# Performance work log

Hardware: AMD Instinct MI355X
Metric: run time of the kernel (lower is better)

## Reference

```python
import jax, jax.numpy as jnp
import numpy as np

N, SD, VD, ED, E, NG, NA, NB = 512, 256, 128, 128, 262144, 16, 16, 5


def _lin_init(key, fan_in, fan_out):
    # torch.nn.Linear default: U(-1/sqrt(fan_in), 1/sqrt(fan_in)); stored as (in, out)
    lim = 1.0 / np.sqrt(fan_in)
    return jax.random.uniform(key, (fan_in, fan_out), jnp.float32, -lim, lim)


def setup_inputs() -> dict:
    key = jax.random.key(0)
    ks = jax.random.split(key, 20)
    s = jax.random.normal(ks[0], (N, SD), jnp.float32)
    v = jax.random.normal(ks[1], (N, 3, VD), jnp.float32)
    p = jax.random.normal(ks[2], (N, 3), jnp.float32)
    e = jax.random.normal(ks[3], (E, ED), jnp.float32)
    batch = jnp.sort(jax.random.randint(ks[4], (N,), 0, NG))
    edge_index_global = jax.random.randint(ks[5], (2, E), 0, N)
    W_sm = _lin_init(ks[6], SD, SD); b_sm = jnp.zeros((SD,), jnp.float32)
    W_bm = _lin_init(ks[7], ED, SD); b_bm = jnp.zeros((SD,), jnp.float32)
    W_b0 = _lin_init(ks[8], SD + 1, SD); b_b0 = jnp.zeros((SD,), jnp.float32)
    W_b1 = _lin_init(ks[9], SD, NB); b_b1 = jnp.zeros((NB,), jnp.float32)
    W_c = _lin_init(ks[10], VD, 1)  # no bias
    W_a = _lin_init(ks[11], SD, NA); b_a = jnp.zeros((NA,), jnp.float32)
    return {"s": s, "v": v, "p": p, "e": e, "batch": batch,
            "edge_index_global": edge_index_global,
            "W_sm": W_sm, "b_sm": b_sm, "W_bm": W_bm, "b_bm": b_bm,
            "W_b0": W_b0, "b_b0": b_b0, "W_b1": W_b1, "b_b1": b_b1,
            "W_c": W_c, "W_a": W_a, "b_a": b_a}


def reference(s, v, p, e, batch, edge_index_global,
              W_sm, b_sm, W_bm, b_bm, W_b0, b_b0, W_b1, b_b1, W_c, W_a, b_a):
    # shared_mapping: Linear + SiLU
    s = jax.nn.silu(s @ W_sm + b_sm)                      # [N, SD]
    coords_pred = (v @ W_c)[..., 0]                       # [N, 3]
    atoms_pred = s @ W_a + b_a                            # [N, NA]
    j, i = edge_index_global[0], edge_index_global[1]
    n = s.shape[0]
    # coords_param == 'data': coords = p + pred, then per-graph mean centering
    coords_pred = p + coords_pred
    seg_sum = jax.ops.segment_sum(coords_pred, batch, num_segments=NG)
    counts = jax.ops.segment_sum(jnp.ones((n, 1), coords_pred.dtype), batch, num_segments=NG)
    mean = seg_sum / jnp.maximum(counts, 1.0)
    coords_pred = coords_pred - mean[batch]
    # squared pairwise distance per edge
    d = jnp.sum((coords_pred[i] - coords_pred[j]) ** 2, axis=-1, keepdims=True)  # [E, 1]
    # sparse -> dense -> sparse symmetrization of edge features (as in the source)
    e_dense = jnp.zeros((n, n, e.shape[-1]), e.dtype).at[j, i].set(e)
    e_dense = 0.5 * (e_dense + jnp.transpose(e_dense, (1, 0, 2)))
    e_sym = e_dense[j, i]                                 # [E, ED]
    f = s[i] + s[j] + (e_sym @ W_bm + b_bm)               # [E, SD]
    edge = jnp.concatenate([f, d], axis=-1)               # [E, SD+1]
    bonds_pred = jax.nn.silu(edge @ W_b0 + b_b0) @ W_b1 + b_b1  # [E, NB]
    return coords_pred, atoms_pred, bonds_pred
```

## Files before the change

### kernel.cpp

```cpp
#include <hip/hip_runtime.h>
#include <math.h>

#define N_NODES 512
#define SD_ 256
#define VD_ 128
#define ED_ 128
#define NE_ 262144
#define NG_ 16
#define NA_ 16
#define NB_ 5
#define MAXP 131328

typedef __attribute__((ext_vector_type(8))) short bf16x8;
typedef __attribute__((ext_vector_type(4))) float f32x4;

__device__ __forceinline__ float silu_f(float x) { return x / (1.0f + expf(-x)); }
__device__ __forceinline__ float silu_fast(float x) {
    return x * __builtin_amdgcn_rcpf(1.0f + __builtin_amdgcn_exp2f(x * -1.44269504f));
}
__device__ __forceinline__ unsigned short f2bf(float x) {
    unsigned int u = __float_as_uint(x);
    return (unsigned short)((u + 0x7fffu + ((u >> 16) & 1u)) >> 16);
}
__device__ __forceinline__ float bf2f(unsigned short h) {
    return __uint_as_float(((unsigned int)h) << 16);
}
__device__ __forceinline__ unsigned int cvt_pk_bf16(float lo, float hi) {
    unsigned int r;
    asm("v_cvt_pk_bf16_f32 %0, %1, %2" : "=v"(r) : "v"(lo), "v"(hi));
    return r;
}

__global__ __launch_bounds__(256) void prep_a(
    const int* __restrict__ ei, int* __restrict__ emap,
    const float* __restrict__ W_bm, const float* __restrict__ W_b0,
    unsigned short* __restrict__ WfF,
    const float* __restrict__ s, const float* __restrict__ v, const float* __restrict__ p,
    const float* __restrict__ W_sm, const float* __restrict__ b_sm,
    const float* __restrict__ W_a, const float* __restrict__ b_a,
    const float* __restrict__ W_c,
    const float* __restrict__ b_bm, const float* __restrict__ b_b0,
    float* __restrict__ s2f, float* __restrict__ cpred, float* __restrict__ atoms_out,
    int* __restrict__ counter, float* __restrict__ zrow, float* __restrict__ bias2)
{
    __shared__ float srow[8][SD_];
    __shared__ float s2row[8][SD_];
    const int bid = blockIdx.x;
    const int tid = threadIdx.x;

    if (bid < 1024) {
        int k = bid * 256 + tid;
        int j = ei[k], i = ei[NE_ + k];
        atomicMax(&emap[j * N_NODES + i], k);
        return;
    }
    if (bid < 1152) {
        int k = bid - 1024;
        srow[0][tid] = W_bm[(size_t)k * SD_ + tid];
        __syncthreads();
        float acc = 0.f;
        #pragma unroll 8
        for (int c = 0; c < SD_; ++c)
            acc = fmaf(srow[0][c], W_b0[(size_t)c * SD_ + tid], acc);
        int mtg = tid >> 4, lo = tid & 15;
        int kb = k >> 5, r = k & 31;
        int l = ((r >> 3) << 4) | lo;
        WfF[((size_t)((mtg * 4 + kb) * 64 + l) << 3) + (r & 7)] = f2bf(acc);
        return;
    }
    if (bid < 1216) {
        const int n0 = (bid - 1152) * 8;
        #pragma unroll
        for (int n = 0; n < 8; ++n) srow[n][tid] = s[(size_t)(n0 + n) * SD_ + tid];
        __syncthreads();
        float acc[8];
        {
            float bb = b_sm[tid];
            #pragma unroll
            for (int n = 0; n < 8; ++n) acc[n] = bb;
        }
        #pragma unroll 4
        for (int c = 0; c < SD_; ++c) {
            float wv = W_sm[(size_t)c * SD_ + tid];
            #pragma unroll
            for (int n = 0; n < 8; ++n) acc[n] = fmaf(srow[n][c], wv, acc[n]);
        }
        #pragma unroll
        for (int n = 0; n < 8; ++n) {
            float sv = silu_f(acc[n]);
            s2f[(size_t)(n0 + n) * SD_ + tid] = sv;
            s2row[n][tid] = sv;
        }
        __syncthreads();
        if (tid < 128) {
            int n = tid >> 4, a = tid & 15;
            float x = b_a[a];
            #pragma unroll 8
            for (int c = 0; c < SD_; ++c) x = fmaf(s2row[n][c], W_a[(size_t)c * NA_ + a], x);
            atoms_out[(size_t)(n0 + n) * NA_ + a] = x;
        }
        return;
    }
    if (bid == 1216) {
        if (tid == 0) counter[0] = 0;
        if (tid < ED_) zrow[tid] = 0.0f;
        for (int o = tid; o < N_NODES * 3; o += 256) {
            float x = p[o];
            const float* vr = v + (size_t)o * VD_;
            #pragma unroll 8
            for (int c = 0; c < VD_; ++c) x = fmaf(vr[c], W_c[c], x);
            cpred[o] = x;
        }
        return;
    }
    {
        float acc = b_b0[tid];
        for (int c = 0; c < SD_; ++c)
            acc = fmaf(b_bm[c], W_b0[(size_t)c * SD_ + tid], acc);
        bias2[tid] = acc;
    }
}

__global__ __launch_bounds__(512) void prep_b(
    const float* __restrict__ cpred, const int* __restrict__ batch,
    float* __restrict__ coords_ws, float* __restrict__ coords_out,
    const int* __restrict__ emap, int* __restrict__ counter,
    int* __restrict__ pairslot, int4* __restrict__ worklist,
    const float* __restrict__ s2f, const float* __restrict__ W_b0,
    float* __restrict__ S2W)
{
    __shared__ float cl[N_NODES * 3];
    __shared__ int   bl[N_NODES];
    __shared__ float meanv[NG_ * 3];
    const int tid = threadIdx.x;
    const int bid = blockIdx.x;

    if (bid == 0) {
        bl[tid] = batch[tid];
        #pragma unroll
        for (int dd = 0; dd < 3; ++dd) cl[tid * 3 + dd] = cpred[tid * 3 + dd];
        __syncthreads();
        if (tid < NG_ * 3) {
            int g = tid / 3, dd = tid % 3;
            float sum = 0.f; int cnt = 0;
            for (int n = 0; n < N_NODES; ++n) {
                if (bl[n] == g) { sum += cl[n * 3 + dd]; cnt++; }
            }
            meanv[tid] = sum / (float)(cnt > 0 ? cnt : 1);
        }
        __syncthreads();
        int g = bl[tid];
        #pragma unroll
        for (int dd = 0; dd < 3; ++dd) {
            float val = cl[tid * 3 + dd] - meanv[g * 3 + dd];
            coords_ws[tid * 3 + dd]  = val;
            coords_out[tid * 3 + dd] = val;
        }
        return;
    }
    if (bid <= 512) {
        int idx = (bid - 1) * 512 + tid;
        int a = idx >> 9, b = idx & (N_NODES - 1);
        bool lower = (a <= b);
        int k1 = -1, k2 = -1;
        if (lower) {
            k1 = emap[(a << 9) | b];
            k2 = emap[(b << 9) | a];
        }
        bool qual = lower && (k1 >= 0 || k2 >= 0);
        unsigned long long mask = __ballot(qual);
        if (mask == 0ull) return;
        int lane = tid & 63;
        int leader = __ffsll((unsigned long long)mask) - 1;
        int base = 0;
        if (lane == leader) base = atomicAdd(counter, __popcll(mask));
        base = __shfl(base, leader);
        if (qual) {
            int slot = base + __popcll(mask & ((1ull << lane) - 1ull));
            pairslot[(a << 9) | b] = slot;
            pairslot[(b << 9) | a] = slot;
            worklist[slot] = make_int4(a, b, k1, k2);
        }
        return;
    }
    {
        __shared__ float srows[2][SD_];
        int n0 = (bid - 513) * 2;
        if (tid < 512) {
            int n = tid >> 8, c = tid & 255;
            srows[n][c] = s2f[(size_t)(n0 + n) * SD_ + c];
        }
        __syncthreads();
        int n = tid >> 8, m = tid & 255;
        float acc = 0.f;
        #pragma unroll 8
        for (int c = 0; c < SD_; ++c)
            acc = fmaf(srows[n][c], W_b0[(size_t)c * SD_ + m], acc);
        S2W[(size_t)(n0 + n) * SD_ + m] = acc;
    }
}

__global__ __launch_bounds__(256) void bonds_scatter(
    const int* __restrict__ ei, const int* __restrict__ pairslot,
    const float* __restrict__ repval, float* __restrict__ bonds_out)
{
    int k = blockIdx.x * 256 + threadIdx.x;
    int j = ei[k], i = ei[NE_ + k];
    int slot = pairslot[(j << 9) | i];
    const float* rp = repval + (size_t)slot * NB_;
    #pragma unroll
    for (int b = 0; b < NB_; ++b)
        bonds_out[(size_t)k * NB_ + b] = rp[b];
}

__global__ __launch_bounds__(512) void edge_mfma(
    const float* __restrict__ e, const int4* __restrict__ worklist,
    const int* __restrict__ counter, const float* __restrict__ coords,
    const float* __restrict__ zrow,
    const unsigned short* __restrict__ WfF, const float* __restrict__ S2W,
    const float* __restrict__ bias2,
    const float* __restrict__ W_b1, const float* __restrict__ W_b0_last,
    const float* __restrict__ b_b1,
    float* __restrict__ repval)
{
    const int blk = blockIdx.x;
    const int cnt = counter[0];
    if (blk * 64 >= cnt) return;

    __shared__ __align__(16) unsigned short esym_lds[64 * 128];
    __shared__ unsigned short wb1t[NB_ * 256];
    __shared__ float bonds_part[8 * 64 * NB_];
    __shared__ float dw[64];
    __shared__ int li_s[64], lj_s[64];

    const int tid = threadIdx.x;
    const int l   = tid & 63;
    const int w   = tid >> 6;
    const int eLo = l & 15;
    const int hi  = l >> 4;

    bf16x8 a1pf[2][2];
    #pragma unroll
    for (int kb = 0; kb < 2; ++kb)
        #pragma unroll
        for (int mt = 0; mt < 2; ++mt)
            a1pf[kb][mt] = *(const bf16x8*)(WfF + ((size_t)(((w * 2 + mt) * 4 + kb) * 64 + l) * 8));

    if (tid < 256) {
        const int rp   = l >> 2;
        const int sub  = l & 3;
        const int pair = w * 16 + rp;
        int widx = min(blk * 64 + pair, cnt - 1);
        int4 wk = worklist[widx];
        const float* r1 = (wk.z >= 0) ? (e + (size_t)wk.z * ED_) : zrow;
        const float* r2 = (wk.w >= 0) ? (e + (size_t)wk.w * ED_) : zrow;
        float4 va[8], vb[8];
        #pragma unroll
        for (int t = 0; t < 8; ++t)
            va[t] = *(const float4*)(r1 + t * 16 + sub * 4);
        #pragma unroll
        for (int t = 0; t < 8; ++t)
            vb[t] = *(const float4*)(r2 + t * 16 + sub * 4);
        #pragma unroll
        for (int t = 0; t < 8; ++t) {
            va[t].x += vb[t].x; va[t].y += vb[t].y;
            va[t].z += vb[t].z; va[t].w += vb[t].w;
        }
        const int ntB = w;
        const int eLoB = rp;
        #pragma unroll
        for (int t = 0; t < 8; ++t) {
            uint2 pk;
            pk.x = cvt_pk_bf16(0.5f * va[t].x, 0.5f * va[t].y);
            pk.y = cvt_pk_bf16(0.5f * va[t].z, 0.5f * va[t].w);
            int kb = t >> 1;
            int h2 = ((t & 1) << 1) | (sub >> 1);
            int chunk = (ntB * 4 + kb) * 64 + h2 * 16 + eLoB;
            *(uint2*)((char*)esym_lds + chunk * 16 + ((sub & 1) << 3)) = pk;
        }
    } else {
        int t = tid - 256;
        #pragma unroll
        for (int b = 0; b < NB_; ++b)
            wb1t[b * 256 + t] = f2bf(W_b1[(size_t)t * NB_ + b]);
        if (t < 64) {
            int widx = min(blk * 64 + t, cnt - 1);
            int4 wk = worklist[widx];
            li_s[t] = wk.x; lj_s[t] = wk.y;
            float dx = coords[wk.x * 3 + 0] - coords[wk.y * 3 + 0];
            float dy = coords[wk.x * 3 + 1] - coords[wk.y * 3 + 1];
            float dz = coords[wk.x * 3 + 2] - coords[wk.y * 3 + 2];
            dw[t] = dx * dx + dy * dy + dz * dz;
        }
    }

    __syncthreads();

    f32x4 acc[2][4];
    #pragma unroll
    for (int mt = 0; mt < 2; ++mt) {
        int m0 = w * 32 + mt * 16 + hi * 4;
        float4 bz = *(const float4*)(bias2 + m0);
        float4 w2 = *(const float4*)(W_b0_last + m0);
        #pragma unroll
        for (int nt = 0; nt < 4; ++nt) {
            int pair = nt * 16 + eLo;
            int na = li_s[pair], nb2 = lj_s[pair];
            float4 sa  = *(const float4*)(S2W + (size_t)na  * SD_ + m0);
            float4 sb4 = *(const float4*)(S2W + (size_t)nb2 * SD_ + m0);
            float dd = dw[pair];
            acc[mt][nt] = (f32x4){fmaf(dd, w2.x, bz.x) + sa.x + sb4.x,
                                  fmaf(dd, w2.y, bz.y) + sa.y + sb4.y,
                                  fmaf(dd, w2.z, bz.z) + sa.z + sb4.z,
                                  fmaf(dd, w2.w, bz.w) + sa.w + sb4.w};
        }
    }

    #pragma unroll
    for (int kb = 0; kb < 4; ++kb) {
        bf16x8 af[2], bfg[4];
        #pragma unroll
        for (int mt = 0; mt < 2; ++mt)
            af[mt] = (kb < 2) ? a1pf[kb][mt]
                   : *(const bf16x8*)(WfF + ((size_t)(((w * 2 + mt) * 4 + kb) * 64 + l) * 8));
        #pragma unroll
        for (int nt = 0; nt < 4; ++nt)
            bfg[nt] = *(const bf16x8*)(&esym_lds[(size_t)((nt * 4 + kb) * 64 + l) * 8]);
        __builtin_amdgcn_s_setprio(1);
        #pragma unroll
        for (int mt = 0; mt < 2; ++mt)
            #pragma unroll
            for (int nt = 0; nt < 4; ++nt)
                acc[mt][nt] = __builtin_amdgcn_mfma_f32_16x16x32_bf16(af[mt], bfg[nt], acc[mt][nt], 0, 0, 0);
        __builtin_amdgcn_s_setprio(0);
    }

    float pb[4][NB_];
    #pragma unroll
    for (int nt = 0; nt < 4; ++nt)
        #pragma unroll
        for (int b = 0; b < NB_; ++b) pb[nt][b] = 0.f;
    #pragma unroll
    for (int mt = 0; mt < 2; ++mt) {
        int m0 = w * 32 + mt * 16 + hi * 4;
        ushort4 wv[NB_];
        #pragma unroll
        for (int b = 0; b < NB_; ++b)
            wv[b] = *(const ushort4*)(wb1t + b * 256 + m0);
        #pragma unroll
        for (int nt = 0; nt < 4; ++nt) {
            f32x4 r = acc[mt][nt];
            float h0 = silu_fast(r[0]);
            float h1 = silu_fast(r[1]);
            float h2 = silu_fast(r[2]);
            float h3 = silu_fast(r[3]);
            #pragma unroll
            for (int b = 0; b < NB_; ++b) {
                float t = fmaf(h0, bf2f(wv[b].x), fmaf(h1, bf2f(wv[b].y),
                          fmaf(h2, bf2f(wv[b].z), h3 * bf2f(wv[b].w))));
                pb[nt][b] += t;
            }
        }
    }
    #pragma unroll
    for (int off = 16; off <= 32; off <<= 1)
        #pragma unroll
        for (int nt = 0; nt < 4; ++nt)
            #pragma unroll
            for (int b = 0; b < NB_; ++b)
                pb[nt][b] += __shfl_xor(pb[nt][b], off);
    if (hi == 0) {
        #pragma unroll
        for (int nt = 0; nt < 4; ++nt)
            #pragma unroll
            for (int b = 0; b < NB_; ++b)
                bonds_part[(size_t)(w * 64 + nt * 16 + eLo) * NB_ + b] = pb[nt][b];
    }
    __syncthreads();

    for (int idx = tid; idx < 64 * NB_; idx += 512) {
        int edge = idx / NB_, b = idx % NB_;
        float s8 = 0.f;
        #pragma unroll
        for (int pp = 0; pp < 8; ++pp)
            s8 += bonds_part[(size_t)(pp * 64 + edge) * NB_ + b];
        repval[(size_t)(blk * 64 + edge) * NB_ + b] = s8 + b_b1[b];
    }
}

extern "C" void kernel_launch(void* const* d_in, const int* in_sizes, int n_in,
                              void* d_out, int out_size, void* d_ws, size_t ws_size,
                              hipStream_t stream)
{
    const float* s    = (const float*)d_in[0];
    const float* v    = (const float*)d_in[1];
    const float* p    = (const float*)d_in[2];
    const float* e    = (const float*)d_in[3];
    const int*   batch= (const int*)d_in[4];
    const int*   ei   = (const int*)d_in[5];
    const float* W_sm = (const float*)d_in[6];
    const float* b_sm = (const float*)d_in[7];
    const float* W_bm = (const float*)d_in[8];
    const float* b_bm = (const float*)d_in[9];
    const float* W_b0 = (const float*)d_in[10];
    const float* b_b0 = (const float*)d_in[11];
    const float* W_b1 = (const float*)d_in[12];
    const float* b_b1 = (const float*)d_in[13];
    const float* W_c  = (const float*)d_in[14];
    const float* W_a  = (const float*)d_in[15];
    const float* b_a  = (const float*)d_in[16];

    float* out = (float*)d_out;
    float* coords_out = out;
    float* atoms_out  = out + 1536;
    float* bonds_out  = out + 1536 + 8192;

    char* ws = (char*)d_ws;
    int*            emap    = (int*)ws;
    float*          s2f     = (float*)(ws + 0x100000);
    unsigned short* WfF     = (unsigned short*)(ws + 0x180000);
    float*          S2W     = (float*)(ws + 0x190000);
    float*          bias2   = (float*)(ws + 0x210000);
    float*          cpred   = (float*)(ws + 0x211000);
    float*          coords  = (float*)(ws + 0x213000);
    int*            counter = (int*)(ws + 0x215000);
    float*          zrow    = (float*)(ws + 0x215100);
    int*            pairslot= (int*)(ws + 0x2A0000);
    int4*           worklist= (int4*)(ws + 0x3A0000);
    float*          repval  = (float*)(ws + 0x5D0000);

    prep_a<<<1218, 256, 0, stream>>>(ei, emap, W_bm, W_b0, WfF,
                                     s, v, p, W_sm, b_sm, W_a, b_a, W_c,
                                     b_bm, b_b0,
                                     s2f, cpred, atoms_out, counter, zrow, bias2);
    prep_b<<<769, 512, 0, stream>>>(cpred, batch, coords, coords_out,
                                    emap, counter, pairslot, worklist,
                                    s2f, W_b0, S2W);

    edge_mfma<<<(MAXP + 63) / 64, 512, 0, stream>>>(e, worklist, counter, coords, zrow,
                                                    WfF, S2W, bias2,
                                                    W_b1, W_b0 + 256 * SD_, b_b1,
                                                    repval);
    bonds_scatter<<<NE_ / 256, 256, 0, stream>>>(ei, pairslot, repval, bonds_out);
}
```

Before: 126.3 us.

## Process two 64-edge tiles per block, prefetching second tile's edge features during first

Each edge_mfma block now handles 128 unique pairs in two 64-pair phases. The upper 256 threads, previously lightly loaded, gather and pack the second tile's symmetrized edge features into registers before the first barrier, then write them into shared memory after the first tile's MFMA. The intent is to hide the global gather latency of the second tile behind the first tile's compute and halve the block count. The cost is extra barriers, more registers per thread (which may lower occupancy), and dropping the weight prefetch registers.

```diff
diff --git a/kernel.cpp b/kernel.cpp
--- a/kernel.cpp
+++ b/kernel.cpp
@@ -225,32 +225,27 @@
 {
     const int blk = blockIdx.x;
     const int cnt = counter[0];
-    if (blk * 64 >= cnt) return;
+    if (blk * 128 >= cnt) return;
 
     __shared__ __align__(16) unsigned short esym_lds[64 * 128];
     __shared__ unsigned short wb1t[NB_ * 256];
     __shared__ float bonds_part[8 * 64 * NB_];
-    __shared__ float dw[64];
-    __shared__ int li_s[64], lj_s[64];
+    __shared__ float dw[128];
+    __shared__ int li_s[128], lj_s[128];
 
     const int tid = threadIdx.x;
     const int l   = tid & 63;
     const int w   = tid >> 6;
     const int eLo = l & 15;
     const int hi  = l >> 4;
-
-    bf16x8 a1pf[2][2];
-    #pragma unroll
-    for (int kb = 0; kb < 2; ++kb)
-        #pragma unroll
-        for (int mt = 0; mt < 2; ++mt)
-            a1pf[kb][mt] = *(const bf16x8*)(WfF + ((size_t)(((w * 2 + mt) * 4 + kb) * 64 + l) * 8));
+    const int rp  = l >> 2;
+    const int sub = l & 3;
+
+    unsigned int t1pk[16];
 
     if (tid < 256) {
-        const int rp   = l >> 2;
-        const int sub  = l & 3;
         const int pair = w * 16 + rp;
-        int widx = min(blk * 64 + pair, cnt - 1);
+        int widx = min(blk * 128 + pair, cnt - 1);
         int4 wk = worklist[widx];
         const float* r1 = (wk.z >= 0) ? (e + (size_t)wk.z * ED_) : zrow;
         const float* r2 = (wk.w >= 0) ? (e + (size_t)wk.w * ED_) : zrow;
@@ -266,8 +261,7 @@
             va[t].x += vb[t].x; va[t].y += vb[t].y;
             va[t].z += vb[t].z; va[t].w += vb[t].w;
         }
-        const int ntB = w;
-        const int eLoB = rp;
+        const int ntB = w, eLoB = rp;
         #pragma unroll
         for (int t = 0; t < 8; ++t) {
             uint2 pk;
@@ -283,8 +277,8 @@
         #pragma unroll
         for (int b = 0; b < NB_; ++b)
             wb1t[b * 256 + t] = f2bf(W_b1[(size_t)t * NB_ + b]);
-        if (t < 64) {
-            int widx = min(blk * 64 + t, cnt - 1);
+        if (t < 128) {
+            int widx = min(blk * 128 + t, cnt - 1);
             int4 wk = worklist[widx];
             li_s[t] = wk.x; lj_s[t] = wk.y;
             float dx = coords[wk.x * 3 + 0] - coords[wk.y * 3 + 0];
@@ -292,11 +286,35 @@
             float dz = coords[wk.x * 3 + 2] - coords[wk.y * 3 + 2];
             dw[t] = dx * dx + dy * dy + dz * dz;
         }
+        const int pair64 = (w - 4) * 16 + rp;
+        int widx1 = min(blk * 128 + 64 + pair64, cnt - 1);
+        int4 wk1 = worklist[widx1];
+        const float* r1 = (wk1.z >= 0) ? (e + (size_t)wk1.z * ED_) : zrow;
+        const float* r2 = (wk1.w >= 0) ? (e + (size_t)wk1.w * ED_) : zrow;
+        float4 va[8], vb[8];
+        #pragma unroll
+        for (int t2 = 0; t2 < 8; ++t2)
+            va[t2] = *(const float4*)(r1 + t2 * 16 + sub * 4);
+        #pragma unroll
+        for (int t2 = 0; t2 < 8; ++t2)
+            vb[t2] = *(const float4*)(r2 + t2 * 16 + sub * 4);
+        #pragma unroll
+        for (int t2 = 0; t2 < 8; ++t2) {
+            va[t2].x += vb[t2].x; va[t2].y += vb[t2].y;
+            va[t2].z += vb[t2].z; va[t2].w += vb[t2].w;
+        }
+        #pragma unroll
+        for (int t2 = 0; t2 < 8; ++t2) {
+            t1pk[2 * t2]     = cvt_pk_bf16(0.5f * va[t2].x, 0.5f * va[t2].y);
+            t1pk[2 * t2 + 1] = cvt_pk_bf16(0.5f * va[t2].z, 0.5f * va[t2].w);
+        }
     }
 
     __syncthreads();
 
     f32x4 acc[2][4];
+    float pb[4][NB_];
+
     #pragma unroll
     for (int mt = 0; mt < 2; ++mt) {
         int m0 = w * 32 + mt * 16 + hi * 4;
@@ -315,14 +333,12 @@
                                   fmaf(dd, w2.w, bz.w) + sa.w + sb4.w};
         }
     }
-
     #pragma unroll
     for (int kb = 0; kb < 4; ++kb) {
         bf16x8 af[2], bfg[4];
         #pragma unroll
         for (int mt = 0; mt < 2; ++mt)
-            af[mt] = (kb < 2) ? a1pf[kb][mt]
-                   : *(const bf16x8*)(WfF + ((size_t)(((w * 2 + mt) * 4 + kb) * 64 + l) * 8));
+            af[mt] = *(const bf16x8*)(WfF + ((size_t)(((w * 2 + mt) * 4 + kb) * 64 + l) * 8));
         #pragma unroll
         for (int nt = 0; nt < 4; ++nt)
             bfg[nt] = *(const bf16x8*)(&esym_lds[(size_t)((nt * 4 + kb) * 64 + l) * 8]);
@@ -334,8 +350,22 @@
                 acc[mt][nt] = __builtin_amdgcn_mfma_f32_16x16x32_bf16(af[mt], bfg[nt], acc[mt][nt], 0, 0, 0);
         __builtin_amdgcn_s_setprio(0);
     }
-
-    float pb[4][NB_];
+    __syncthreads();
+
+    if (tid >= 256) {
+        const int ntB = w - 4, eLoB = rp;
+        #pragma unroll
+        for (int t2 = 0; t2 < 8; ++t2) {
+            uint2 pk;
+            pk.x = t1pk[2 * t2];
+            pk.y = t1pk[2 * t2 + 1];
+            int kb = t2 >> 1;
+            int h2 = ((t2 & 1) << 1) | (sub >> 1);
+            int chunk = (ntB * 4 + kb) * 64 + h2 * 16 + eLoB;
+            *(uint2*)((char*)esym_lds + chunk * 16 + ((sub & 1) << 3)) = pk;
+        }
+    }
+
     #pragma unroll
     for (int nt = 0; nt < 4; ++nt)
         #pragma unroll
@@ -384,7 +414,96 @@
         #pragma unroll
         for (int pp = 0; pp < 8; ++pp)
             s8 += bonds_part[(size_t)(pp * 64 + edge) * NB_ + b];
-        repval[(size_t)(blk * 64 + edge) * NB_ + b] = s8 + b_b1[b];
+        repval[(size_t)(blk * 128 + edge) * NB_ + b] = s8 + b_b1[b];
+    }
+
+    #pragma unroll
+    for (int mt = 0; mt < 2; ++mt) {
+        int m0 = w * 32 + mt * 16 + hi * 4;
+        float4 bz = *(const float4*)(bias2 + m0);
+        float4 w2 = *(const float4*)(W_b0_last + m0);
+        #pragma unroll
+        for (int nt = 0; nt < 4; ++nt) {
+            int pair = 64 + nt * 16 + eLo;
+            int na = li_s[pair], nb2 = lj_s[pair];
+            float4 sa  = *(const float4*)(S2W + (size_t)na  * SD_ + m0);
+            float4 sb4 = *(const float4*)(S2W + (size_t)nb2 * SD_ + m0);
+            float dd = dw[pair];
+            acc[mt][nt] = (f32x4){fmaf(dd, w2.x, bz.x) + sa.x + sb4.x,
+                                  fmaf(dd, w2.y, bz.y) + sa.y + sb4.y,
+                                  fmaf(dd, w2.z, bz.z) + sa.z + sb4.z,
+                                  fmaf(dd, w2.w, bz.w) + sa.w + sb4.w};
+        }
+    }
+    #pragma unroll
+    for (int kb = 0; kb < 4; ++kb) {
+        bf16x8 af[2], bfg[4];
+        #pragma unroll
+        for (int mt = 0; mt < 2; ++mt)
+            af[mt] = *(const bf16x8*)(WfF + ((size_t)(((w * 2 + mt) * 4 + kb) * 64 + l) * 8));
+        #pragma unroll
+        for (int nt = 0; nt < 4; ++nt)
+            bfg[nt] = *(const bf16x8*)(&esym_lds[(size_t)((nt * 4 + kb) * 64 + l) * 8]);
+        __builtin_amdgcn_s_setprio(1);
+        #pragma unroll
+        for (int mt = 0; mt < 2; ++mt)
+            #pragma unroll
+            for (int nt = 0; nt < 4; ++nt)
+                acc[mt][nt] = __builtin_amdgcn_mfma_f32_16x16x32_bf16(af[mt], bfg[nt], acc[mt][nt], 0, 0, 0);
+        __builtin_amdgcn_s_setprio(0);
+    }
+
+    #pragma unroll
+    for (int nt = 0; nt < 4; ++nt)
+        #pragma unroll
+        for (int b = 0; b < NB_; ++b) pb[nt][b] = 0.f;
+    #pragma unroll
+    for (int mt = 0; mt < 2; ++mt) {
+        int m0 = w * 32 + mt * 16 + hi * 4;
+        ushort4 wv[NB_];
+        #pragma unroll
+        for (int b = 0; b < NB_; ++b)
+            wv[b] = *(const ushort4*)(wb1t + b * 256 + m0);
+        #pragma unroll
+        for (int nt = 0; nt < 4; ++nt) {
+            f32x4 r = acc[mt][nt];
+            float h0 = silu_fast(r[0]);
+            float h1 = silu_fast(r[1]);
+            float h2 = silu_fast(r[2]);
+            float h3 = silu_fast(r[3]);
+            #pragma unroll
+            for (int b = 0; b < NB_; ++b) {
+                float t = fmaf(h0, bf2f(wv[b].x), fmaf(h1, bf2f(wv[b].y),
+                          fmaf(h2, bf2f(wv[b].z), h3 * bf2f(wv[b].w))));
+                pb[nt][b] += t;
+            }
+        }
+    }
+    #pragma unroll
+    for (int off = 16; off <= 32; off <<= 1)
+        #pragma unroll
+        for (int nt = 0; nt < 4; ++nt)
+            #pragma unroll
+            for (int b = 0; b < NB_; ++b)
+                pb[nt][b] += __shfl_xor(pb[nt][b], off);
+
+    __syncthreads();
+    if (hi == 0) {
+        #pragma unroll
+        for (int nt = 0; nt < 4; ++nt)
+            #pragma unroll
+            for (int b = 0; b < NB_; ++b)
+                bonds_part[(size_t)(w * 64 + nt * 16 + eLo) * NB_ + b] = pb[nt][b];
+    }
+    __syncthreads();
+
+    for (int idx = tid; idx < 64 * NB_; idx += 512) {
+        int edge = idx / NB_, b = idx % NB_;
+        float s8 = 0.f;
+        #pragma unroll
+        for (int pp = 0; pp < 8; ++pp)
+            s8 += bonds_part[(size_t)(pp * 64 + edge) * NB_ + b];
+        repval[(size_t)(blk * 128 + 64 + edge) * NB_ + b] = s8 + b_b1[b];
     }
 }
 
@@ -437,9 +556,9 @@
                                     emap, counter, pairslot, worklist,
                                     s2f, W_b0, S2W);
 
-    edge_mfma<<<(MAXP + 63) / 64, 512, 0, stream>>>(e, worklist, counter, coords, zrow,
-                                                    WfF, S2W, bias2,
-                                                    W_b1, W_b0 + 256 * SD_, b_b1,
-                                                    repval);
+    edge_mfma<<<(MAXP + 127) / 128, 512, 0, stream>>>(e, worklist, counter, coords, zrow,
+                                                      WfF, S2W, bias2,
+                                                      W_b1, W_b0 + 256 * SD_, b_b1,
+                                                      repval);
     bonds_scatter<<<NE_ / 256, 256, 0, stream>>>(ei, pairslot, repval, bonds_out);
 }
```

Result: slower. 134.4 us (+6.5%).
